# Kernel tuning notes

Hardware: AMD Instinct MI355X
Metric: run time of the kernel (lower is better)

Reference implementation:

```python
import jax, jax.numpy as jnp
import numpy as np

NEG = -1000000.0  # mask fill value used by the original sequence_mask


def setup_inputs() -> dict:
    key = jax.random.key(0)
    k1, k2, k3, k4 = jax.random.split(key, 4)
    B, Nq, Nk, D = 8, 2048, 2048, 64
    queries = jax.random.normal(k1, (B, Nq, D), dtype=jnp.float32)
    keys = jax.random.normal(k2, (B, Nk, D), dtype=jnp.float32)
    values = jax.random.normal(k3, (B, Nk, D), dtype=jnp.float32)
    valid_lens = jax.random.randint(k4, (B,), 1, Nk + 1, dtype=jnp.int32)
    return {"queries": queries, "keys": keys, "values": values, "valid_lens": valid_lens}


def reference(queries, keys, values, valid_lens):
    d = queries.shape[-1]
    # scores: (B, n_q, n_k)
    scores = jnp.einsum("bqd,bkd->bqk", queries, keys) / jnp.sqrt(jnp.float32(d))
    # mask key positions >= valid_len (per-batch valid length, broadcast over queries)
    nk = scores.shape[-1]
    key_pos = jnp.arange(nk, dtype=jnp.int32)  # (n_k,)
    mask = key_pos[None, None, :] < valid_lens[:, None, None]  # (B, 1->n_q, n_k)
    scores = jnp.where(mask, scores, NEG)
    attn = jax.nn.softmax(scores, axis=-1)
    # dropout is identity in inference mode (no training flag in the original call)
    return jnp.einsum("bqk,bkd->bqd", attn, values)
```

## Files before the change

### kernel.cpp

```cpp
#include <hip/hip_runtime.h>
#include <hip/hip_bf16.h>


typedef __attribute__((ext_vector_type(8))) short bf16x8;
typedef __attribute__((ext_vector_type(8))) unsigned short u16x8;
typedef __attribute__((ext_vector_type(4))) float f32x4;

#define NQ 2048
#define NK 2048
#define DH 64
#define NB 8
#define NSPLIT 16
#define SPLIT_LEN 128
#define L2E 1.44269504088896341f
#define PSTRIDE 36

#define VMCNT(n) asm volatile("s_waitcnt vmcnt(" #n ")" ::: "memory")

__device__ __forceinline__ unsigned short f2bf(float f) {
    union { float f; unsigned int u; } v; v.f = f;
    unsigned int u = v.u;
    u += 0x7FFFu + ((u >> 16) & 1u);
    return (unsigned short)(u >> 16);
}
__device__ __forceinline__ float bf2f(unsigned short u) {
    union { unsigned int u; float f; } v; v.u = ((unsigned int)u) << 16; return v.f;
}
__device__ __forceinline__ unsigned int pack_bf2(float lo, float hi) {
    return ((unsigned int)f2bf(hi) << 16) | (unsigned int)f2bf(lo);
}
__device__ __forceinline__ float fast_exp2(float x) {
#if __has_builtin(__builtin_amdgcn_exp2f)
    return __builtin_amdgcn_exp2f(x);
#else
    return exp2f(x);
#endif
}
__device__ __forceinline__ void gload16(const void* g, void* l) {
    __builtin_amdgcn_global_load_lds(
        (const __attribute__((address_space(1))) void*)g,
        (__attribute__((address_space(3))) void*)l, 16, 0, 0);
}

__global__ __launch_bounds__(256) void prep(const float* __restrict__ K,
                                            const float* __restrict__ Q,
                                            const float* __restrict__ V,
                                            unsigned short* __restrict__ Kbf,
                                            unsigned short* __restrict__ Qbf,
                                            unsigned short* __restrict__ Vt) {
    if (blockIdx.x < 1024) {
        const bool isQ = blockIdx.x >= 512;
        const size_t idx = ((size_t)(blockIdx.x & 511) * 256 + threadIdx.x) * 8;
        const float* src = isQ ? Q : K;
        const float sc = isQ ? 0.125f : 1.0f;
        const float4 a = *reinterpret_cast<const float4*>(src + idx);
        const float4 b = *reinterpret_cast<const float4*>(src + idx + 4);
        bf16x8 o;
        o[0] = (short)f2bf(a.x * sc); o[1] = (short)f2bf(a.y * sc);
        o[2] = (short)f2bf(a.z * sc); o[3] = (short)f2bf(a.w * sc);
        o[4] = (short)f2bf(b.x * sc); o[5] = (short)f2bf(b.y * sc);
        o[6] = (short)f2bf(b.z * sc); o[7] = (short)f2bf(b.w * sc);
        *reinterpret_cast<bf16x8*>((isQ ? Qbf : Kbf) + idx) = o;
    } else {
        __shared__ unsigned short T[64][65];
        const int bid2 = blockIdx.x - 1024;
        const int b  = bid2 >> 5;
        const int k0 = (bid2 & 31) * 64;
        const int t  = threadIdx.x;
        const int r  = t >> 2;
        const int cb = (t & 3) * 16;
        const float* src = V + ((size_t)(b * NK + k0 + r)) * DH + cb;
#pragma unroll
        for (int j4 = 0; j4 < 4; ++j4) {
            const float4 v = *reinterpret_cast<const float4*>(src + j4 * 4);
            T[r][cb + j4 * 4 + 0] = f2bf(v.x);
            T[r][cb + j4 * 4 + 1] = f2bf(v.y);
            T[r][cb + j4 * 4 + 2] = f2bf(v.z);
            T[r][cb + j4 * 4 + 3] = f2bf(v.w);
        }
        __syncthreads();
        unsigned short* dstb = Vt + (size_t)b * DH * NK;
#pragma unroll
        for (int i = 0; i < 2; ++i) {
            const int cc = t + i * 256;
            const int d  = cc >> 3;
            const int kb = (cc & 7) * 8;
            bf16x8 o;
#pragma unroll
            for (int j = 0; j < 8; ++j) o[j] = (short)T[kb + j][d];
            *reinterpret_cast<bf16x8*>(dstb + (size_t)d * NK + k0 + kb) = o;
        }
    }
}

__global__ __launch_bounds__(512, 6) void attn_split(
    const unsigned short* __restrict__ Qbf, const unsigned short* __restrict__ Kbf,
    const unsigned short* __restrict__ Vt, const int* __restrict__ VL,
    float* __restrict__ Lsum, unsigned short* __restrict__ Opart)
{
    __shared__ __align__(16) unsigned char KV[32768];
    __shared__ __align__(16) unsigned int Pl[8][16 * PSTRIDE];

    const int bid = blockIdx.x;
    const int x   = bid & 7;
    const int k   = bid >> 3;
    const int qg  = k & 15;
    const int cs  = k >> 4;
    const int b   = cs & 7;
    const int s   = ((x - b) & 7) + (cs >> 3) * 8;

    const int vlen  = VL[b];
    const int kv_lo = s * SPLIT_LEN;
    if (kv_lo >= vlen) return;
    const int kv_hi = min(vlen, kv_lo + SPLIT_LEN);
    const int chunk = kv_hi - kv_lo;

    const int tid  = threadIdx.x;
    const int wv   = tid >> 6;
    const int lane = tid & 63;
    const int g = lane >> 4;
    const int c = lane & 15;
    const int qt = qg * 8 + wv;
    const int swl = (c & 7) << 4;

    const unsigned short* Qb = Qbf + ((size_t)b * NQ + qt * 16) * DH;
    const unsigned char* Kc = (const unsigned char*)(Kbf + ((size_t)b * NK + kv_lo) * DH);
    const unsigned char* Vbase = (const unsigned char*)(Vt + (size_t)b * DH * NK);
    const int vk0b = kv_lo * 2;
    unsigned int* Pw = &Pl[wv][0];

#pragma unroll
    for (int i = 0; i < 2; ++i) {
        const int p = i * 8192 + tid * 16;
        const int a = p ^ (((p >> 7) & 7) << 4);
        gload16(Kc + a, KV + p);
    }
#pragma unroll
    for (int i = 0; i < 2; ++i) {
        const int p = i * 8192 + tid * 16;
        const int a = p ^ (((p >> 8) & 7) << 4);
        const int d  = a >> 8;
        const int ko = a & 255;
        gload16(Vbase + (size_t)d * (NK * 2) + vk0b + ko, KV + 16384 + p);
    }

    bf16x8 qf[2];
#pragma unroll
    for (int ks = 0; ks < 2; ++ks)
        qf[ks] = *reinterpret_cast<const bf16x8*>(Qb + (size_t)c * DH + ks * 32 + g * 8);

    f32x4 acc[4];
#pragma unroll
    for (int i = 0; i < 4; ++i) acc[i] = (f32x4){0.f, 0.f, 0.f, 0.f};
    float l_run = 0.f;

    VMCNT(0);
    __builtin_amdgcn_s_barrier();
    __builtin_amdgcn_sched_barrier(0);

    const int ntt = (chunk + 63) >> 6;
    for (int tt = 0; tt < ntt; ++tt) {
        const int kv0 = kv_lo + (tt << 6);

        f32x4 sv[4];
#pragma unroll
        for (int nt4 = 0; nt4 < 4; ++nt4) {
            const int aK = (tt * 64 + nt4 * 16 + c) * 128 + g * 16;
            const bf16x8 kf0 = *reinterpret_cast<const bf16x8*>(KV + (aK ^ swl));
            const bf16x8 kf1 = *reinterpret_cast<const bf16x8*>(KV + ((aK + 64) ^ swl));
            f32x4 tacc = (f32x4){0.f, 0.f, 0.f, 0.f};
            tacc = __builtin_amdgcn_mfma_f32_16x16x32_bf16(kf0, qf[0], tacc, 0, 0, 0);
            tacc = __builtin_amdgcn_mfma_f32_16x16x32_bf16(kf1, qf[1], tacc, 0, 0, 0);
            sv[nt4] = tacc;
        }

        bf16x8 vf[2][4];
#pragma unroll
        for (int ks2 = 0; ks2 < 2; ++ks2)
#pragma unroll
            for (int ntd = 0; ntd < 4; ++ntd) {
                const int aV = (ntd * 16 + c) * 256 + tt * 128 + ks2 * 64 + g * 16;
                vf[ks2][ntd] = *reinterpret_cast<const bf16x8*>(KV + 16384 + (aV ^ swl));
            }

        if (kv0 + 64 > kv_hi) {
#pragma unroll
            for (int nt4 = 0; nt4 < 4; ++nt4)
#pragma unroll
                for (int r = 0; r < 4; ++r)
                    if (kv0 + nt4 * 16 + 4 * g + r >= vlen) sv[nt4][r] = -1e30f;
        }

        float rs = 0.f;
#pragma unroll
        for (int nt4 = 0; nt4 < 4; ++nt4)
#pragma unroll
            for (int r = 0; r < 4; ++r) {
                const float p = fast_exp2(sv[nt4][r] * L2E);
                sv[nt4][r] = p;
                rs += p;
            }
        l_run += rs;

#pragma unroll
        for (int nt4 = 0; nt4 < 4; ++nt4) {
            Pw[c * PSTRIDE + nt4 * 8 + 2 * g]     = pack_bf2(sv[nt4][0], sv[nt4][1]);
            Pw[c * PSTRIDE + nt4 * 8 + 2 * g + 1] = pack_bf2(sv[nt4][2], sv[nt4][3]);
        }
        asm volatile("s_waitcnt lgkmcnt(0)" ::: "memory");
        const bf16x8 pa0 = *reinterpret_cast<const bf16x8*>(&Pw[c * PSTRIDE + 4 * g]);
        const bf16x8 pa1 = *reinterpret_cast<const bf16x8*>(&Pw[c * PSTRIDE + 16 + 4 * g]);

#pragma unroll
        for (int ntd = 0; ntd < 4; ++ntd)
            acc[ntd] = __builtin_amdgcn_mfma_f32_16x16x32_bf16(pa0, vf[0][ntd], acc[ntd], 0, 0, 0);
#pragma unroll
        for (int ntd = 0; ntd < 4; ++ntd)
            acc[ntd] = __builtin_amdgcn_mfma_f32_16x16x32_bf16(pa1, vf[1][ntd], acc[ntd], 0, 0, 0);
    }

    float lf = l_run;
    lf += __shfl_xor(lf, 16);
    lf += __shfl_xor(lf, 32);

    const size_t pbase = (size_t)(b * NSPLIT + s) * 128 + qt;
    if (lane < 16) Lsum[pbase * 16 + c] = lf;

    u16x8 pk0, pk1;
#pragma unroll
    for (int ntd = 0; ntd < 2; ++ntd)
#pragma unroll
        for (int r = 0; r < 4; ++r) pk0[ntd * 4 + r] = f2bf(acc[ntd][r]);
#pragma unroll
    for (int ntd = 2; ntd < 4; ++ntd)
#pragma unroll
        for (int r = 0; r < 4; ++r) pk1[(ntd - 2) * 4 + r] = f2bf(acc[ntd][r]);
    unsigned short* op = Opart + pbase * 1024 + (size_t)lane * 16;
    *reinterpret_cast<u16x8*>(op)     = pk0;
    *reinterpret_cast<u16x8*>(op + 8) = pk1;
}

__global__ __launch_bounds__(256) void attn_merge(
    const float* __restrict__ Lsum, const unsigned short* __restrict__ Opart,
    const int* __restrict__ VL, float* __restrict__ O)
{
    const int tid  = threadIdx.x;
    const int wv   = tid >> 6;
    const int lane = tid & 63;
    const int g = lane >> 4;
    const int c = lane & 15;
    const int qi = blockIdx.x * 4 + wv;
    const int b  = qi >> 7;
    const int qt = qi & 127;
    const int vlen = VL[b];
    const int nact = min(NSPLIT, (vlen + SPLIT_LEN - 1) / SPLIT_LEN);

    float accv[16];
    float L4[4] = {0.f, 0.f, 0.f, 0.f};
#pragma unroll
    for (int j = 0; j < 16; ++j) accv[j] = 0.f;

    for (int s = 0; s < nact; ++s) {
        const size_t pb = (size_t)(b * NSPLIT + s) * 128 + qt;
        const u16x8* src = reinterpret_cast<const u16x8*>(
            Opart + pb * 1024 + (size_t)lane * 16);
        const u16x8 lo = src[0], hi = src[1];
#pragma unroll
        for (int j = 0; j < 8; ++j) {
            accv[j]     += bf2f(lo[j]);
            accv[8 + j] += bf2f(hi[j]);
        }
        const float* Lp = Lsum + pb * 16 + 4 * g;
#pragma unroll
        for (int r = 0; r < 4; ++r) L4[r] += Lp[r];
    }
    float inv4[4];
#pragma unroll
    for (int r = 0; r < 4; ++r) inv4[r] = 1.0f / L4[r];

    float* Ob = O + ((size_t)(b * NQ + qt * 16)) * DH;
#pragma unroll
    for (int ntd = 0; ntd < 4; ++ntd)
#pragma unroll
        for (int r = 0; r < 4; ++r)
            Ob[(size_t)(4 * g + r) * DH + ntd * 16 + c] = accv[ntd * 4 + r] * inv4[r];
}

__global__ __launch_bounds__(64) void attn_fwd(
    const float* __restrict__ Q, const float* __restrict__ K,
    const float* __restrict__ V, const int* __restrict__ VL,
    float* __restrict__ O)
{
    __shared__ __align__(16) unsigned short Plds[16 * 40];
    const int bid = blockIdx.x;
    const int b  = bid >> 7;
    const int qt = bid & 127;
    const int q0 = qt * 16;
    const int lane = threadIdx.x;
    const int g = lane >> 4;
    const int c = lane & 15;
    const float* Qb = Q + ((size_t)b * NQ + q0) * DH;
    const float* Kb = K + (size_t)b * NK * DH;
    const float* Vb = V + (size_t)b * NK * DH;
    const int vlen = VL[b];
    bf16x8 qf[2];
#pragma unroll
    for (int ks = 0; ks < 2; ++ks) {
        const float* src = Qb + (size_t)c * DH + ks * 32 + g * 8;
#pragma unroll
        for (int e = 0; e < 8; ++e) qf[ks][e] = (short)f2bf(src[e] * 0.125f);
    }
    f32x4 acc[4];
#pragma unroll
    for (int nt = 0; nt < 4; ++nt) acc[nt] = (f32x4){0.f,0.f,0.f,0.f};
    float m_run[4], l_run[4];
#pragma unroll
    for (int r = 0; r < 4; ++r) { m_run[r] = -3.0e38f; l_run[r] = 0.f; }
    const int ntiles = (vlen + 31) / 32;
    for (int kt = 0; kt < ntiles; ++kt) {
        const int kv0 = kt * 32;
        f32x4 s[2] = {{0.f,0.f,0.f,0.f},{0.f,0.f,0.f,0.f}};
#pragma unroll
        for (int nt = 0; nt < 2; ++nt) {
            const float* kp = Kb + (size_t)(kv0 + nt * 16 + c) * DH + g * 8;
#pragma unroll
            for (int ks = 0; ks < 2; ++ks) {
                bf16x8 kf;
#pragma unroll
                for (int e = 0; e < 8; ++e) kf[e] = (short)f2bf(kp[ks * 32 + e]);
                s[nt] = __builtin_amdgcn_mfma_f32_16x16x32_bf16(qf[ks], kf, s[nt], 0, 0, 0);
            }
        }
        const bool msk0 = (kv0 + c)      >= vlen;
        const bool msk1 = (kv0 + 16 + c) >= vlen;
#pragma unroll
        for (int r = 0; r < 4; ++r) {
            if (msk0) s[0][r] = -1e30f;
            if (msk1) s[1][r] = -1e30f;
        }
        float tmax[4];
#pragma unroll
        for (int r = 0; r < 4; ++r) tmax[r] = fmaxf(s[0][r], s[1][r]);
#pragma unroll
        for (int mbit = 1; mbit < 16; mbit <<= 1)
#pragma unroll
            for (int r = 0; r < 4; ++r)
                tmax[r] = fmaxf(tmax[r], __shfl_xor(tmax[r], mbit));
        float p0[4], p1[4];
#pragma unroll
        for (int r = 0; r < 4; ++r) {
            const float mn = fmaxf(m_run[r], tmax[r]);
            const float sc = fast_exp2((m_run[r] - mn) * L2E);
            m_run[r] = mn;
            p0[r] = fast_exp2((s[0][r] - mn) * L2E);
            p1[r] = fast_exp2((s[1][r] - mn) * L2E);
            l_run[r] = l_run[r] * sc + p0[r] + p1[r];
#pragma unroll
            for (int nt = 0; nt < 4; ++nt) acc[nt][r] *= sc;
        }
#pragma unroll
        for (int r = 0; r < 4; ++r) {
            Plds[(4 * g + r) * 40 + c]      = f2bf(p0[r]);
            Plds[(4 * g + r) * 40 + 16 + c] = f2bf(p1[r]);
        }
        asm volatile("s_waitcnt lgkmcnt(0)" ::: "memory");
        const bf16x8 pa = *reinterpret_cast<const bf16x8*>(&Plds[c * 40 + g * 8]);
#pragma unroll
        for (int nt = 0; nt < 4; ++nt) {
            bf16x8 vf;
#pragma unroll
            for (int e = 0; e < 8; ++e)
                vf[e] = (short)f2bf(Vb[(size_t)(kv0 + 8 * g + e) * DH + nt * 16 + c]);
            acc[nt] = __builtin_amdgcn_mfma_f32_16x16x32_bf16(pa, vf, acc[nt], 0, 0, 0);
        }
    }
#pragma unroll
    for (int mbit = 1; mbit < 16; mbit <<= 1)
#pragma unroll
        for (int r = 0; r < 4; ++r)
            l_run[r] += __shfl_xor(l_run[r], mbit);
    float* Ob = O + ((size_t)b * NQ + q0) * DH;
#pragma unroll
    for (int r = 0; r < 4; ++r) {
        const float inv = 1.0f / l_run[r];
#pragma unroll
        for (int nt = 0; nt < 4; ++nt)
            Ob[(size_t)(4 * g + r) * DH + nt * 16 + c] = acc[nt][r] * inv;
    }
}

extern "C" void kernel_launch(void* const* d_in, const int* in_sizes, int n_in,
                              void* d_out, int out_size, void* d_ws, size_t ws_size,
                              hipStream_t stream) {
    const float* Q  = (const float*)d_in[0];
    const float* K  = (const float*)d_in[1];
    const float* V  = (const float*)d_in[2];
    const int*   VL = (const int*)d_in[3];
    float* O = (float*)d_out;

    const size_t KB_OFF = 0;
    const size_t QB_OFF = (size_t)2 << 20;
    const size_t VT_OFF = (size_t)4 << 20;
    const size_t ML_OFF = (size_t)6 << 20;
    const size_t OP_OFF = (size_t)8 << 20;
    const size_t NEED   = OP_OFF + (size_t)NB * NSPLIT * 128 * 1024 * 2;

    if (ws_size >= NEED) {
        char* w = (char*)d_ws;
        unsigned short* Kbf   = (unsigned short*)(w + KB_OFF);
        unsigned short* Qbf   = (unsigned short*)(w + QB_OFF);
        unsigned short* Vtp   = (unsigned short*)(w + VT_OFF);
        float*          Lsum  = (float*)(w + ML_OFF);
        unsigned short* Opart = (unsigned short*)(w + OP_OFF);

        prep<<<1280, 256, 0, stream>>>(K, Q, V, Kbf, Qbf, Vtp);
        attn_split<<<NB * NSPLIT * 16, 512, 0, stream>>>(Qbf, Kbf, Vtp, VL, Lsum, Opart);
        attn_merge<<<256, 256, 0, stream>>>(Lsum, Opart, VL, O);
    } else {
        attn_fwd<<<NB * 128, 64, 0, stream>>>(Q, K, V, VL, O);
    }
}
```

Baseline: 36.58 us.

## Overlap V load with QK, alias P scratch into K region, raise occupancy

Merges the K/V tile and per-wave P scratch into one shared buffer, placing seven waves' P scratch over the K region (already consumed) and the eighth in a small tail, which cuts LDS per block. It waits only for the K loads before computing both QK tiles, then waits for V, so the V transfer overlaps with QK work. Launch bounds rise from 6 to 8 blocks to use the smaller LDS footprint, and V fragments are loaded just before use to reduce register pressure. The loop is specialised to at most two 64-key tiles, matching the 128-key split, and overlapping P over K relies on the barrier ordering being correct.

```diff
diff --git a/kernel.cpp b/kernel.cpp
--- a/kernel.cpp
+++ b/kernel.cpp
@@ -93,13 +93,12 @@
     }
 }
 
-__global__ __launch_bounds__(512, 6) void attn_split(
+__global__ __launch_bounds__(512, 8) void attn_split(
     const unsigned short* __restrict__ Qbf, const unsigned short* __restrict__ Kbf,
     const unsigned short* __restrict__ Vt, const int* __restrict__ VL,
     float* __restrict__ Lsum, unsigned short* __restrict__ Opart)
 {
-    __shared__ __align__(16) unsigned char KV[32768];
-    __shared__ __align__(16) unsigned int Pl[8][16 * PSTRIDE];
+    __shared__ __align__(16) unsigned char MEM[32768 + 2304];
 
     const int bid = blockIdx.x;
     const int x   = bid & 7;
@@ -127,13 +126,18 @@
     const unsigned char* Kc = (const unsigned char*)(Kbf + ((size_t)b * NK + kv_lo) * DH);
     const unsigned char* Vbase = (const unsigned char*)(Vt + (size_t)b * DH * NK);
     const int vk0b = kv_lo * 2;
-    unsigned int* Pw = &Pl[wv][0];
-
+    unsigned int* Pw = (unsigned int*)(wv < 7 ? MEM + wv * (PSTRIDE * 16 * 4)
+                                              : MEM + 32768);
+
+    bf16x8 qf[2];
+#pragma unroll
+    for (int ks = 0; ks < 2; ++ks)
+        qf[ks] = *reinterpret_cast<const bf16x8*>(Qb + (size_t)c * DH + ks * 32 + g * 8);
 #pragma unroll
     for (int i = 0; i < 2; ++i) {
         const int p = i * 8192 + tid * 16;
         const int a = p ^ (((p >> 7) & 7) << 4);
-        gload16(Kc + a, KV + p);
+        gload16(Kc + a, MEM + p);
     }
 #pragma unroll
     for (int i = 0; i < 2; ++i) {
@@ -141,48 +145,30 @@
         const int a = p ^ (((p >> 8) & 7) << 4);
         const int d  = a >> 8;
         const int ko = a & 255;
-        gload16(Vbase + (size_t)d * (NK * 2) + vk0b + ko, KV + 16384 + p);
-    }
-
-    bf16x8 qf[2];
-#pragma unroll
-    for (int ks = 0; ks < 2; ++ks)
-        qf[ks] = *reinterpret_cast<const bf16x8*>(Qb + (size_t)c * DH + ks * 32 + g * 8);
-
-    f32x4 acc[4];
-#pragma unroll
-    for (int i = 0; i < 4; ++i) acc[i] = (f32x4){0.f, 0.f, 0.f, 0.f};
-    float l_run = 0.f;
-
-    VMCNT(0);
+        gload16(Vbase + (size_t)d * (NK * 2) + vk0b + ko, MEM + 16384 + p);
+    }
+
+    const int ntt = (chunk + 63) >> 6;
+
+    VMCNT(2);
     __builtin_amdgcn_s_barrier();
     __builtin_amdgcn_sched_barrier(0);
 
-    const int ntt = (chunk + 63) >> 6;
-    for (int tt = 0; tt < ntt; ++tt) {
-        const int kv0 = kv_lo + (tt << 6);
-
+    float l_run = 0.f;
+
+    auto qk_tile = [&](int tt, unsigned int* pk) {
         f32x4 sv[4];
 #pragma unroll
         for (int nt4 = 0; nt4 < 4; ++nt4) {
             const int aK = (tt * 64 + nt4 * 16 + c) * 128 + g * 16;
-            const bf16x8 kf0 = *reinterpret_cast<const bf16x8*>(KV + (aK ^ swl));
-            const bf16x8 kf1 = *reinterpret_cast<const bf16x8*>(KV + ((aK + 64) ^ swl));
+            const bf16x8 kf0 = *reinterpret_cast<const bf16x8*>(MEM + (aK ^ swl));
+            const bf16x8 kf1 = *reinterpret_cast<const bf16x8*>(MEM + ((aK + 64) ^ swl));
             f32x4 tacc = (f32x4){0.f, 0.f, 0.f, 0.f};
             tacc = __builtin_amdgcn_mfma_f32_16x16x32_bf16(kf0, qf[0], tacc, 0, 0, 0);
             tacc = __builtin_amdgcn_mfma_f32_16x16x32_bf16(kf1, qf[1], tacc, 0, 0, 0);
             sv[nt4] = tacc;
         }
-
-        bf16x8 vf[2][4];
-#pragma unroll
-        for (int ks2 = 0; ks2 < 2; ++ks2)
-#pragma unroll
-            for (int ntd = 0; ntd < 4; ++ntd) {
-                const int aV = (ntd * 16 + c) * 256 + tt * 128 + ks2 * 64 + g * 16;
-                vf[ks2][ntd] = *reinterpret_cast<const bf16x8*>(KV + 16384 + (aV ^ swl));
-            }
-
+        const int kv0 = kv_lo + (tt << 6);
         if (kv0 + 64 > kv_hi) {
 #pragma unroll
             for (int nt4 = 0; nt4 < 4; ++nt4)
@@ -190,7 +176,6 @@
                 for (int r = 0; r < 4; ++r)
                     if (kv0 + nt4 * 16 + 4 * g + r >= vlen) sv[nt4][r] = -1e30f;
         }
-
         float rs = 0.f;
 #pragma unroll
         for (int nt4 = 0; nt4 < 4; ++nt4)
@@ -201,23 +186,49 @@
                 rs += p;
             }
         l_run += rs;
-
 #pragma unroll
         for (int nt4 = 0; nt4 < 4; ++nt4) {
-            Pw[c * PSTRIDE + nt4 * 8 + 2 * g]     = pack_bf2(sv[nt4][0], sv[nt4][1]);
-            Pw[c * PSTRIDE + nt4 * 8 + 2 * g + 1] = pack_bf2(sv[nt4][2], sv[nt4][3]);
+            pk[nt4 * 2]     = pack_bf2(sv[nt4][0], sv[nt4][1]);
+            pk[nt4 * 2 + 1] = pack_bf2(sv[nt4][2], sv[nt4][3]);
+        }
+    };
+
+    unsigned int pkA[8], pkB[8];
+    qk_tile(0, pkA);
+    if (ntt > 1) qk_tile(1, pkB);
+
+    VMCNT(0);
+    __builtin_amdgcn_s_barrier();
+    __builtin_amdgcn_sched_barrier(0);
+
+    f32x4 acc[4];
+#pragma unroll
+    for (int i = 0; i < 4; ++i) acc[i] = (f32x4){0.f, 0.f, 0.f, 0.f};
+
+    auto pv_tile = [&](int tt, const unsigned int* pk) {
+#pragma unroll
+        for (int nt4 = 0; nt4 < 4; ++nt4) {
+            Pw[c * PSTRIDE + nt4 * 8 + 2 * g]     = pk[nt4 * 2];
+            Pw[c * PSTRIDE + nt4 * 8 + 2 * g + 1] = pk[nt4 * 2 + 1];
         }
         asm volatile("s_waitcnt lgkmcnt(0)" ::: "memory");
         const bf16x8 pa0 = *reinterpret_cast<const bf16x8*>(&Pw[c * PSTRIDE + 4 * g]);
         const bf16x8 pa1 = *reinterpret_cast<const bf16x8*>(&Pw[c * PSTRIDE + 16 + 4 * g]);
-
-#pragma unroll
-        for (int ntd = 0; ntd < 4; ++ntd)
-            acc[ntd] = __builtin_amdgcn_mfma_f32_16x16x32_bf16(pa0, vf[0][ntd], acc[ntd], 0, 0, 0);
-#pragma unroll
-        for (int ntd = 0; ntd < 4; ++ntd)
-            acc[ntd] = __builtin_amdgcn_mfma_f32_16x16x32_bf16(pa1, vf[1][ntd], acc[ntd], 0, 0, 0);
-    }
+#pragma unroll
+        for (int ks2 = 0; ks2 < 2; ++ks2) {
+            const bf16x8 pa = ks2 ? pa1 : pa0;
+#pragma unroll
+            for (int ntd = 0; ntd < 4; ++ntd) {
+                const int aV = (ntd * 16 + c) * 256 + tt * 128 + ks2 * 64 + g * 16;
+                const bf16x8 vf = *reinterpret_cast<const bf16x8*>(MEM + 16384 + (aV ^ swl));
+                acc[ntd] = __builtin_amdgcn_mfma_f32_16x16x32_bf16(pa, vf, acc[ntd], 0, 0, 0);
+            }
+        }
+        asm volatile("s_waitcnt lgkmcnt(0)" ::: "memory");
+    };
+
+    pv_tile(0, pkA);
+    if (ntt > 1) pv_tile(1, pkB);
 
     float lf = l_run;
     lf += __shfl_xor(lf, 16);
```

After: 32.12 us. -12.2%, faster.
